# Performance work log

Hardware: AMD Instinct MI355X
Metric: run time of the kernel (lower is better)

Reference implementation:

```python
import jax, jax.numpy as jnp
import numpy as np

N, S = 65536, 2048        # dense points, sampled centres
D1, D2 = 64, 256          # skip-feature dim, centre-embedding dim
MLP = [256, 128]          # conv1x1 channel stack
BN_EPS = 1e-5             # flax BatchNorm default
INTERP_EPS = 1e-8


def setup_inputs() -> dict:
    key = jax.random.key(0)
    ks = jax.random.split(key, 6)
    inp = {
        "xyz1": jax.random.normal(ks[0], (3, N), jnp.float32),
        "xyz2": jax.random.normal(ks[1], (3, S), jnp.float32),
        "points1": jax.random.normal(ks[2], (D1, N), jnp.float32),
        "points2": jax.random.normal(ks[3], (D2, S), jnp.float32),
    }
    c_in = D1 + D2
    for i, c_out in enumerate(MLP):
        inp[f"w{i}"] = jax.random.normal(ks[4 + i], (c_in, c_out), jnp.float32) / np.float32(np.sqrt(c_in))
        inp[f"b{i}"] = jnp.zeros((c_out,), jnp.float32)
        inp[f"scale{i}"] = jnp.ones((c_out,), jnp.float32)
        inp[f"bias{i}"] = jnp.zeros((c_out,), jnp.float32)
        inp[f"mean{i}"] = jnp.zeros((c_out,), jnp.float32)   # BN running mean
        inp[f"var{i}"] = jnp.ones((c_out,), jnp.float32)     # BN running var
        c_in = c_out
    return inp


def reference(xyz1, xyz2, points1, points2,
              w0, b0, scale0, bias0, mean0, var0,
              w1, b1, scale1, bias1, mean1, var1):
    x1 = xyz1.T            # [N, 3]
    x2 = xyz2.T            # [S, 3]
    p2 = points2.T         # [S, D2]

    # squared pairwise distances [N, S]
    dists = (jnp.sum(x1 * x1, -1, keepdims=True)
             + jnp.sum(x2 * x2, -1)[None, :]
             - 2.0 * (x1 @ x2.T))

    # 3 nearest neighbours (smallest dist) per dense point
    neg_d3, idx = jax.lax.top_k(-dists, 3)      # [N, 3]
    d3 = -neg_d3
    recip = 1.0 / (d3 + INTERP_EPS)
    w = recip / jnp.sum(recip, axis=1, keepdims=True)   # [N, 3]

    # inverse-distance-weighted interpolation: [N, D2]
    interp = jnp.einsum('nkd,nk->nd', p2[idx], w)

    new = jnp.concatenate([points1.T, interp], axis=-1)  # [N, D1+D2]

    # conv1x1 (== dense) + BN (inference, running stats) + ReLU stack
    for W, b, s, bb, m, v in ((w0, b0, scale0, bias0, mean0, var0),
                              (w1, b1, scale1, bias1, mean1, var1)):
        y = new @ W + b
        y = (y - m) * (s / jnp.sqrt(v + BN_EPS)) + bb
        new = jax.nn.relu(y)

    return new.T           # [MLP[-1], N]
```

## Files before the change

### kernel.cpp

```cpp
#include <hip/hip_runtime.h>
#include <math.h>

#define NPTS 65536
#define NS   2048
#define C2   256
#define C3   128

#define WS_P2T     32768
#define WS_W0F     1081344
#define WS_W1F     1245184
#define WS_AB0     1310720
#define WS_AB1     1312768
#define WS_KIDX    1313792
#define WS_KW      2100224

typedef __attribute__((ext_vector_type(8))) short bf16x8;
typedef __attribute__((ext_vector_type(4))) float f32x4;

__device__ __forceinline__ unsigned short f2bf(float f) {
  unsigned u = __builtin_bit_cast(unsigned, f);
  u = (u + 0x7FFFu + ((u >> 16) & 1u)) >> 16;
  return (unsigned short)u;
}
__device__ __forceinline__ float bf2f(unsigned h) {
  return __builtin_bit_cast(float, h << 16);
}

__global__ __launch_bounds__(256) void pnfp_knn(
    const float* __restrict__ xyz1, const float* __restrict__ xyz2,
    const float* __restrict__ points2,
    const float* __restrict__ w0, const float* __restrict__ b0,
    const float* __restrict__ scale0, const float* __restrict__ bias0,
    const float* __restrict__ mean0, const float* __restrict__ var0,
    const float* __restrict__ w1, const float* __restrict__ b1,
    const float* __restrict__ scale1, const float* __restrict__ bias1,
    const float* __restrict__ mean1, const float* __restrict__ var1,
    unsigned char* __restrict__ ws)
{
  __shared__ __align__(16) unsigned char kns[33024];
  const int tid = threadIdx.x;

  if (blockIdx.x >= 1024) {
    const int pbid = blockIdx.x - 1024;
    if (pbid < 128) {
      float (*tile)[65] = (float(*)[65])kns;
      const int st = pbid & 31, dt = pbid >> 5;
#pragma unroll
      for (int it = 0; it < 16; ++it) {
        int j = it * 256 + tid;
        int d = j >> 6, s = j & 63;
        tile[d][s] = points2[(dt * 64 + d) * NS + st * 64 + s];
      }
      __syncthreads();
      unsigned short* p2t = (unsigned short*)(ws + WS_P2T);
#pragma unroll
      for (int it = 0; it < 16; ++it) {
        int j = it * 256 + tid;
        int s = j >> 6, d = j & 63;
        p2t[(st * 64 + s) * 256 + dt * 64 + d] = f2bf(tile[d][s]);
      }
      return;
    }
    int gid = (pbid - 128) * 256 + tid;
    if (gid < 81920) {
      int i = gid & 7, l = (gid >> 3) & 63, c = (gid >> 9) & 15, ks = gid >> 13;
      int k = ks * 32 + (l >> 4) * 8 + i;
      int col = c * 16 + (l & 15);
      ((unsigned short*)(ws + WS_W0F))[gid] = f2bf(w0[k * C2 + col]);
      return;
    }
    gid -= 81920;
    if (gid < 32768) {
      int i = gid & 7, l = (gid >> 3) & 63, c = (gid >> 9) & 7, ks = gid >> 12;
      int k = ks * 32 + (l >> 4) * 8 + i;
      int col = c * 16 + (l & 15);
      ((unsigned short*)(ws + WS_W1F))[gid] = f2bf(w1[k * C3 + col]);
      return;
    }
    gid -= 32768;
    if (gid < 256) {
      float a = scale0[gid] / sqrtf(var0[gid] + 1e-5f);
      float bb = (b0[gid] - mean0[gid]) * a + bias0[gid];
      float* ab = (float*)(ws + WS_AB0);
      ab[gid] = a; ab[256 + gid] = bb;
      return;
    }
    gid -= 256;
    if (gid < 128) {
      float a = scale1[gid] / sqrtf(var1[gid] + 1e-5f);
      float bb = (b1[gid] - mean1[gid]) * a + bias1[gid];
      float* ab = (float*)(ws + WS_AB1);
      ab[gid] = a; ab[128 + gid] = bb;
    }
    return;
  }

  float4* cs = (float4*)kns;
  for (int j = tid; j < NS; j += 256) {
    float x = xyz2[j], y = xyz2[NS + j], z = xyz2[2 * NS + j];
    float sc;
    {
#pragma clang fp contract(off)
      sc = (x * x + y * y) + z * z;
    }
    cs[(j >> 7) * 129 + (j & 127)] = make_float4(x, y, z, sc);
  }
  __syncthreads();

  const int rank = tid & 15;
  const int set = tid >> 4;
  const int nb = blockIdx.x * 64 + set * 4;

  float px[4], py[4], pz[4], ps[4];
#pragma unroll
  for (int p = 0; p < 4; ++p) {
    int n = nb + p;
    px[p] = xyz1[n]; py[p] = xyz1[NPTS + n]; pz[p] = xyz1[2 * NPTS + n];
    {
#pragma clang fp contract(off)
      ps[p] = (px[p] * px[p] + py[p] * py[p]) + pz[p] * pz[p];
    }
  }

  float D0[4], D1[4], D2[4];
  int I0[4], I1[4], I2[4];
#pragma unroll
  for (int p = 0; p < 4; ++p) {
    D0[p] = 1e30f; D1[p] = 1e30f; D2[p] = 1e30f;
    I0[p] = 0; I1[p] = 0; I2[p] = 0;
  }

  const float4* cq = cs + rank * 129;
  const int sbase = rank << 7;
#pragma unroll 4
  for (int t = 0; t < 128; ++t) {
    const float4 c = cq[t];
    const int s = sbase + t;
#pragma unroll
    for (int p = 0; p < 4; ++p) {
      float dot = fmaf(pz[p], c.z, fmaf(py[p], c.y, px[p] * c.x));
      float d = (ps[p] + c.w) - 2.0f * dot;
      const bool c2 = d < D2[p], c1 = d < D1[p], c0 = d < D0[p];
      I2[p] = c2 ? (c1 ? I1[p] : s) : I2[p];
      I1[p] = c1 ? (c0 ? I0[p] : s) : I1[p];
      I0[p] = c0 ? s : I0[p];
      float n1 = __builtin_amdgcn_fmed3f(D0[p], D1[p], d);
      float n2 = __builtin_amdgcn_fmed3f(D1[p], D2[p], d);
      D0[p] = fminf(D0[p], d);
      D1[p] = n1; D2[p] = n2;
    }
  }

#pragma unroll
  for (int p = 0; p < 4; ++p) {
#pragma unroll
    for (int m = 1; m <= 8; m <<= 1) {
      float e0 = __shfl_xor(D0[p], m), e1 = __shfl_xor(D1[p], m), e2 = __shfl_xor(D2[p], m);
      int  j0 = __shfl_xor(I0[p], m), j1 = __shfl_xor(I1[p], m), j2 = __shfl_xor(I2[p], m);
      bool t0 = e0 < D0[p];
      float r0 = t0 ? e0 : D0[p]; int ri0 = t0 ? j0 : I0[p];
      float X0 = t0 ? D0[p] : D1[p], X1 = t0 ? D1[p] : D2[p];
      int  XI0 = t0 ? I0[p] : I1[p], XI1 = t0 ? I1[p] : I2[p];
      float Y0 = t0 ? e1 : e0, Y1v = t0 ? e2 : e1;
      int  YJ0 = t0 ? j1 : j0, YJ1 = t0 ? j2 : j1;
      bool t1 = Y0 < X0;
      float r1 = t1 ? Y0 : X0; int ri1 = t1 ? YJ0 : XI0;
      float X0b = t1 ? X0 : X1; int XI0b = t1 ? XI0 : XI1;
      float Y0b = t1 ? Y1v : Y0; int YJ0b = t1 ? YJ1 : YJ0;
      bool t2 = Y0b < X0b;
      float r2 = t2 ? Y0b : X0b; int ri2 = t2 ? YJ0b : XI0b;
      D0[p] = r0; D1[p] = r1; D2[p] = r2; I0[p] = ri0; I1[p] = ri1; I2[p] = ri2;
    }
  }

  if (rank == 0) {
#pragma unroll
    for (int p = 0; p < 4; ++p) {
      const int n = nb + p;
      float q0 = 1.0f / (D0[p] + 1e-8f);
      float q1 = 1.0f / (D1[p] + 1e-8f);
      float q2 = 1.0f / (D2[p] + 1e-8f);
      float qs = (q0 + q1) + q2;
      int* oi = (int*)(ws + WS_KIDX) + 3 * n;
      float* owp = (float*)(ws + WS_KW) + 3 * n;
      oi[0] = I0[p]; oi[1] = I1[p]; oi[2] = I2[p];
      owp[0] = q0 / qs; owp[1] = q1 / qs; owp[2] = q2 / qs;
    }
  }
}

__global__ __launch_bounds__(256, 3) void pnfp_fused(
    const float* __restrict__ points1,
    const unsigned char* __restrict__ ws,
    float* __restrict__ out)
{
  __shared__ __align__(16) unsigned char smem[43520];
  unsigned short* Fh = (unsigned short*)smem;
  int*   kI = (int*)(smem + 41984);
  float* kW = (float*)(smem + 42752);
  const unsigned short* p2t = (const unsigned short*)(ws + WS_P2T);
  const unsigned short* w0f = (const unsigned short*)(ws + WS_W0F);
  const unsigned short* w1f = (const unsigned short*)(ws + WS_W1F);
  const float* ab0 = (const float*)(ws + WS_AB0);
  const float* ab1 = (const float*)(ws + WS_AB1);
  const int* kidx = (const int*)(ws + WS_KIDX);
  const float* kw = (const float*)(ws + WS_KW);

  const int tid = threadIdx.x;
  const int wv = tid >> 6, lane = tid & 63;
  const int n0 = blockIdx.x * 64;

  if (tid < 192) {
    kI[tid] = kidx[3 * n0 + tid];
    kW[tid] = kw[3 * n0 + tid];
  }
#pragma unroll
  for (int it = 0; it < 16; ++it) {
    int j = tid + it * 256;
    int d = j >> 6, r = j & 63;
    Fh[r * 328 + d] = f2bf(points1[d * NPTS + n0 + r]);
  }
  __syncthreads();
  {
    const int dbase = lane * 4;
#pragma unroll 4
    for (int rr = 0; rr < 16; ++rr) {
      const int r = wv * 16 + rr;
      const int a0 = kI[3 * r], a1 = kI[3 * r + 1], a2 = kI[3 * r + 2];
      const float w0 = kW[3 * r], w1 = kW[3 * r + 1], w2 = kW[3 * r + 2];
      uint2 u0 = *(const uint2*)(p2t + a0 * 256 + dbase);
      uint2 u1 = *(const uint2*)(p2t + a1 * 256 + dbase);
      uint2 u2 = *(const uint2*)(p2t + a2 * 256 + dbase);
      float f0 = fmaf(w2, bf2f(u2.x & 0xFFFFu), fmaf(w1, bf2f(u1.x & 0xFFFFu), w0 * bf2f(u0.x & 0xFFFFu)));
      float f1 = fmaf(w2, bf2f(u2.x >> 16),     fmaf(w1, bf2f(u1.x >> 16),     w0 * bf2f(u0.x >> 16)));
      float f2v = fmaf(w2, bf2f(u2.y & 0xFFFFu), fmaf(w1, bf2f(u1.y & 0xFFFFu), w0 * bf2f(u0.y & 0xFFFFu)));
      float f3 = fmaf(w2, bf2f(u2.y >> 16),     fmaf(w1, bf2f(u1.y >> 16),     w0 * bf2f(u0.y >> 16)));
      uint2 pk;
      pk.x = (unsigned)f2bf(f0) | ((unsigned)f2bf(f1) << 16);
      pk.y = (unsigned)f2bf(f2v) | ((unsigned)f2bf(f3) << 16);
      *(uint2*)(Fh + r * 328 + 64 + dbase) = pk;
    }
  }
  __syncthreads();

  f32x4 zero4 = {0.f, 0.f, 0.f, 0.f};
  f32x4 acc[4][4];
#pragma unroll
  for (int a = 0; a < 4; ++a)
#pragma unroll
    for (int b = 0; b < 4; ++b) acc[a][b] = zero4;

  const int arow = lane & 15;
  const int koff = (lane >> 4) * 8;
  bf16x8 bcur[4], bnxt[4];
#pragma unroll
  for (int ct = 0; ct < 4; ++ct)
    bcur[ct] = *(const bf16x8*)(w0f + ((wv * 4 + ct) * 64 + lane) * 8);
  for (int ks = 0; ks < 10; ++ks) {
#pragma unroll
    for (int ct = 0; ct < 4; ++ct)
      bnxt[ct] = *(const bf16x8*)(w0f + (((ks + 1) * 16 + wv * 4 + ct) * 64 + lane) * 8);
    bf16x8 af[4];
#pragma unroll
    for (int rt = 0; rt < 4; ++rt)
      af[rt] = *(const bf16x8*)(Fh + (rt * 16 + arow) * 328 + ks * 32 + koff);
#pragma unroll
    for (int ct = 0; ct < 4; ++ct)
#pragma unroll
      for (int rt = 0; rt < 4; ++rt)
        acc[rt][ct] = __builtin_amdgcn_mfma_f32_16x16x32_bf16(af[rt], bcur[ct], acc[rt][ct], 0, 0, 0);
#pragma unroll
    for (int ct = 0; ct < 4; ++ct) bcur[ct] = bnxt[ct];
  }
  __syncthreads();

  unsigned short* Y1 = (unsigned short*)smem;
#pragma unroll
  for (int ct = 0; ct < 4; ++ct) {
    const int c = wv * 64 + ct * 16 + arow;
    const float a = ab0[c], b = ab0[256 + c];
#pragma unroll
    for (int rt = 0; rt < 4; ++rt) {
      const int rbase = rt * 16 + (lane >> 4) * 4;
#pragma unroll
      for (int qi = 0; qi < 4; ++qi) {
        float yv = fmaxf(fmaf(acc[rt][ct][qi], a, b), 0.0f);
        Y1[(rbase + qi) * 264 + c] = f2bf(yv);
      }
    }
  }
  __syncthreads();

  f32x4 acc2[4][2];
#pragma unroll
  for (int a = 0; a < 4; ++a) { acc2[a][0] = zero4; acc2[a][1] = zero4; }
  bf16x8 b2cur[2], b2nxt[2];
#pragma unroll
  for (int ct = 0; ct < 2; ++ct)
    b2cur[ct] = *(const bf16x8*)(w1f + ((wv * 2 + ct) * 64 + lane) * 8);
  for (int ks = 0; ks < 8; ++ks) {
#pragma unroll
    for (int ct = 0; ct < 2; ++ct)
      b2nxt[ct] = *(const bf16x8*)(w1f + (((ks + 1) * 8 + wv * 2 + ct) * 64 + lane) * 8);
    bf16x8 af[4];
#pragma unroll
    for (int rt = 0; rt < 4; ++rt)
      af[rt] = *(const bf16x8*)(Y1 + (rt * 16 + arow) * 264 + ks * 32 + koff);
#pragma unroll
    for (int ct = 0; ct < 2; ++ct)
#pragma unroll
      for (int rt = 0; rt < 4; ++rt)
        acc2[rt][ct] = __builtin_amdgcn_mfma_f32_16x16x32_bf16(af[rt], b2cur[ct], acc2[rt][ct], 0, 0, 0);
#pragma unroll
    for (int ct = 0; ct < 2; ++ct) b2cur[ct] = b2nxt[ct];
  }
  __syncthreads();

  float* OUT = (float*)smem;
#pragma unroll
  for (int ct = 0; ct < 2; ++ct) {
    const int c = wv * 32 + ct * 16 + arow;
    const float a = ab1[c], b = ab1[128 + c];
#pragma unroll
    for (int rt = 0; rt < 4; ++rt) {
      const int rbase = rt * 16 + (lane >> 4) * 4;
#pragma unroll
      for (int qi = 0; qi < 4; ++qi)
        OUT[c * 67 + rbase + qi] = fmaxf(fmaf(acc2[rt][ct][qi], a, b), 0.0f);
    }
  }
  __syncthreads();
#pragma unroll
  for (int it = 0; it < 32; ++it) {
    int j = tid + it * 256;
    int c = j >> 6, n = j & 63;
    out[c * NPTS + n0 + n] = OUT[c * 67 + n];
  }
}

extern "C" void kernel_launch(void* const* d_in, const int* in_sizes, int n_in,
                              void* d_out, int out_size, void* d_ws, size_t ws_size,
                              hipStream_t stream) {
  (void)in_sizes; (void)n_in; (void)out_size; (void)ws_size;
  const float* xyz1    = (const float*)d_in[0];
  const float* xyz2    = (const float*)d_in[1];
  const float* points1 = (const float*)d_in[2];
  const float* points2 = (const float*)d_in[3];
  const float* w0      = (const float*)d_in[4];
  const float* b0      = (const float*)d_in[5];
  const float* scale0  = (const float*)d_in[6];
  const float* bias0   = (const float*)d_in[7];
  const float* mean0   = (const float*)d_in[8];
  const float* var0    = (const float*)d_in[9];
  const float* w1      = (const float*)d_in[10];
  const float* b1      = (const float*)d_in[11];
  const float* scale1  = (const float*)d_in[12];
  const float* bias1   = (const float*)d_in[13];
  const float* mean1   = (const float*)d_in[14];
  const float* var1    = (const float*)d_in[15];
  unsigned char* ws = (unsigned char*)d_ws;
  float* out = (float*)d_out;

  pnfp_knn<<<1602, 256, 0, stream>>>(xyz1, xyz2, points2,
                                     w0, b0, scale0, bias0, mean0, var0,
                                     w1, b1, scale1, bias1, mean1, var1, ws);
  pnfp_fused<<<1024, 256, 0, stream>>>(points1, ws, out);
}
```

Baseline: 204.9 us.

## Replace brute-force kNN with spatial grid search plus exact fallback

Centres are bucketed into a 10x10x10 grid whose cell edges sit at normal-distribution quantiles. Each dense point then searches only its 3x3x3 neighbouring cells and accepts the result when the third-nearest distance lies within the guaranteed bound to the search-region boundary. Points that fail the check go onto a list and get a wave-per-point brute-force search in a fallback kernel. This is meant to remove most of the O(N*S) distance work, at the cost of extra launches, an atomic-built list, a serial single-block sort, and cell boundaries tuned to Gaussian-distributed inputs.

Measured after the change: 384.9 us. 87.8% more time.

```diff
diff --git a/kernel.cpp b/kernel.cpp
--- a/kernel.cpp
+++ b/kernel.cpp
@@ -6,6 +6,7 @@
 #define C2   256
 #define C3   128
 
+#define WS_SORT    0
 #define WS_P2T     32768
 #define WS_W0F     1081344
 #define WS_W1F     1245184
@@ -13,6 +14,10 @@
 #define WS_AB1     1312768
 #define WS_KIDX    1313792
 #define WS_KW      2100224
+#define WS_CSTART  2886656
+#define WS_SIDX    2888704
+#define WS_FCNT    2892800
+#define WS_FLIST   2892816
 
 typedef __attribute__((ext_vector_type(8))) short bf16x8;
 typedef __attribute__((ext_vector_type(4))) float f32x4;
@@ -26,9 +31,48 @@
   return __builtin_bit_cast(float, h << 16);
 }
 
-__global__ __launch_bounds__(256) void pnfp_knn(
-    const float* __restrict__ xyz1, const float* __restrict__ xyz2,
-    const float* __restrict__ points2,
+#define GE0 -1.2815516f
+#define GE1 -0.84162123f
+#define GE2 -0.52440051f
+#define GE3 -0.25334710f
+#define GE4  0.0f
+#define GE5  0.25334710f
+#define GE6  0.52440051f
+#define GE7  0.84162123f
+#define GE8  1.2815516f
+
+__device__ __forceinline__ int cls9(float v) {
+  int c = 0;
+  c += v > GE0; c += v > GE1; c += v > GE2; c += v > GE3; c += v > GE4;
+  c += v > GE5; c += v > GE6; c += v > GE7; c += v > GE8;
+  return c;
+}
+__device__ __forceinline__ void axis_info(float v, int& c, float& blo, float& bhi) {
+  float lom1 = -3e30f, lom2 = -3e30f, him1 = 3e30f, him2 = 3e30f;
+  int cc = 0; bool b;
+  b = v > GE0; cc += b; lom2 = b ? lom1 : lom2; lom1 = b ? GE0 : lom1;
+  b = v > GE1; cc += b; lom2 = b ? lom1 : lom2; lom1 = b ? GE1 : lom1;
+  b = v > GE2; cc += b; lom2 = b ? lom1 : lom2; lom1 = b ? GE2 : lom1;
+  b = v > GE3; cc += b; lom2 = b ? lom1 : lom2; lom1 = b ? GE3 : lom1;
+  b = v > GE4; cc += b; lom2 = b ? lom1 : lom2; lom1 = b ? GE4 : lom1;
+  b = v > GE5; cc += b; lom2 = b ? lom1 : lom2; lom1 = b ? GE5 : lom1;
+  b = v > GE6; cc += b; lom2 = b ? lom1 : lom2; lom1 = b ? GE6 : lom1;
+  b = v > GE7; cc += b; lom2 = b ? lom1 : lom2; lom1 = b ? GE7 : lom1;
+  b = v > GE8; cc += b; lom2 = b ? lom1 : lom2; lom1 = b ? GE8 : lom1;
+  b = !(v > GE8); him2 = b ? him1 : him2; him1 = b ? GE8 : him1;
+  b = !(v > GE7); him2 = b ? him1 : him2; him1 = b ? GE7 : him1;
+  b = !(v > GE6); him2 = b ? him1 : him2; him1 = b ? GE6 : him1;
+  b = !(v > GE5); him2 = b ? him1 : him2; him1 = b ? GE5 : him1;
+  b = !(v > GE4); him2 = b ? him1 : him2; him1 = b ? GE4 : him1;
+  b = !(v > GE3); him2 = b ? him1 : him2; him1 = b ? GE3 : him1;
+  b = !(v > GE2); him2 = b ? him1 : him2; him1 = b ? GE2 : him1;
+  b = !(v > GE1); him2 = b ? him1 : him2; him1 = b ? GE1 : him1;
+  b = !(v > GE0); him2 = b ? him1 : him2; him1 = b ? GE0 : him1;
+  c = cc; blo = v - lom2; bhi = him2 - v;
+}
+
+__global__ __launch_bounds__(256) void pnfp_prep(
+    const float* __restrict__ xyz2, const float* __restrict__ points2,
     const float* __restrict__ w0, const float* __restrict__ b0,
     const float* __restrict__ scale0, const float* __restrict__ bias0,
     const float* __restrict__ mean0, const float* __restrict__ var0,
@@ -37,65 +81,196 @@
     const float* __restrict__ mean1, const float* __restrict__ var1,
     unsigned char* __restrict__ ws)
 {
-  __shared__ __align__(16) unsigned char kns[33024];
+  __shared__ __align__(16) unsigned char psh[49152];
   const int tid = threadIdx.x;
 
-  if (blockIdx.x >= 1024) {
-    const int pbid = blockIdx.x - 1024;
-    if (pbid < 128) {
-      float (*tile)[65] = (float(*)[65])kns;
-      const int st = pbid & 31, dt = pbid >> 5;
-#pragma unroll
-      for (int it = 0; it < 16; ++it) {
-        int j = it * 256 + tid;
-        int d = j >> 6, s = j & 63;
-        tile[d][s] = points2[(dt * 64 + d) * NS + st * 64 + s];
+  if (blockIdx.x < 128) {
+    float (*tile)[65] = (float(*)[65])psh;
+    const int st = blockIdx.x & 31, dt = blockIdx.x >> 5;
+#pragma unroll
+    for (int it = 0; it < 16; ++it) {
+      int j = it * 256 + tid;
+      int d = j >> 6, s = j & 63;
+      tile[d][s] = points2[(dt * 64 + d) * NS + st * 64 + s];
+    }
+    __syncthreads();
+    unsigned short* p2t = (unsigned short*)(ws + WS_P2T);
+#pragma unroll
+    for (int it = 0; it < 16; ++it) {
+      int j = it * 256 + tid;
+      int s = j >> 6, d = j & 63;
+      p2t[(st * 64 + s) * 256 + dt * 64 + d] = f2bf(tile[d][s]);
+    }
+    return;
+  }
+
+  if (blockIdx.x == 578) {
+    float4* cbuf = (float4*)psh;
+    unsigned short* cellid = (unsigned short*)(psh + 32768);
+    unsigned* A  = (unsigned*)(psh + 36864);
+    unsigned* B  = (unsigned*)(psh + 40960);
+    unsigned* og = (unsigned*)(psh + 45056);
+    for (int i = tid; i < 1024; i += 256) A[i] = 0;
+    __syncthreads();
+#pragma unroll
+    for (int k = 0; k < 8; ++k) {
+      int j = tid + k * 256;
+      float x = xyz2[j], y = xyz2[NS + j], z = xyz2[2 * NS + j];
+      float sc;
+      {
+#pragma clang fp contract(off)
+        sc = (x * x + y * y) + z * z;
+      }
+      cbuf[j] = make_float4(x, y, z, sc);
+      int cell = (cls9(z) * 10 + cls9(y)) * 10 + cls9(x);
+      cellid[j] = (unsigned short)cell;
+      atomicAdd(&A[cell], 1u);
+    }
+    __syncthreads();
+    for (int i = tid; i < 1024; i += 256) og[i] = A[i];
+    __syncthreads();
+    unsigned* src = A; unsigned* dst = B;
+    for (int off = 1; off < 1024; off <<= 1) {
+#pragma unroll
+      for (int k = 0; k < 4; ++k) {
+        int i = tid + k * 256;
+        unsigned v = src[i];
+        if (i >= off) v += src[i - off];
+        dst[i] = v;
       }
       __syncthreads();
-      unsigned short* p2t = (unsigned short*)(ws + WS_P2T);
-#pragma unroll
-      for (int it = 0; it < 16; ++it) {
-        int j = it * 256 + tid;
-        int s = j >> 6, d = j & 63;
-        p2t[(st * 64 + s) * 256 + dt * 64 + d] = f2bf(tile[d][s]);
+      unsigned* t = src; src = dst; dst = t;
+    }
+    unsigned short* cst = (unsigned short*)(ws + WS_CSTART);
+    for (int i = tid; i <= 1000; i += 256)
+      cst[i] = (i == 0) ? 0 : (unsigned short)src[i - 1];
+    for (int i = tid; i < 1024; i += 256) og[i] = src[i] - og[i];
+    __syncthreads();
+    float4* so = (float4*)(ws + WS_SORT);
+    unsigned short* sid = (unsigned short*)(ws + WS_SIDX);
+#pragma unroll
+    for (int k = 0; k < 8; ++k) {
+      int j = tid + k * 256;
+      int cell = cellid[j];
+      unsigned pos = atomicAdd(&og[cell], 1u);
+      so[pos] = cbuf[j];
+      sid[pos] = (unsigned short)j;
+    }
+    if (tid == 0) *(unsigned*)(ws + WS_FCNT) = 0u;
+    return;
+  }
+
+  int gid = ((int)blockIdx.x - 128) * 256 + tid;
+  if (gid < 81920) {
+    int i = gid & 7, l = (gid >> 3) & 63, c = (gid >> 9) & 15, ks = gid >> 13;
+    int k = ks * 32 + (l >> 4) * 8 + i;
+    int col = c * 16 + (l & 15);
+    ((unsigned short*)(ws + WS_W0F))[gid] = f2bf(w0[k * C2 + col]);
+    return;
+  }
+  gid -= 81920;
+  if (gid < 32768) {
+    int i = gid & 7, l = (gid >> 3) & 63, c = (gid >> 9) & 7, ks = gid >> 12;
+    int k = ks * 32 + (l >> 4) * 8 + i;
+    int col = c * 16 + (l & 15);
+    ((unsigned short*)(ws + WS_W1F))[gid] = f2bf(w1[k * C3 + col]);
+    return;
+  }
+  gid -= 32768;
+  if (gid < 256) {
+    float a = scale0[gid] / sqrtf(var0[gid] + 1e-5f);
+    float bb = (b0[gid] - mean0[gid]) * a + bias0[gid];
+    float* ab = (float*)(ws + WS_AB0);
+    ab[gid] = a; ab[256 + gid] = bb;
+    return;
+  }
+  gid -= 256;
+  if (gid < 128) {
+    float a = scale1[gid] / sqrtf(var1[gid] + 1e-5f);
+    float bb = (b1[gid] - mean1[gid]) * a + bias1[gid];
+    float* ab = (float*)(ws + WS_AB1);
+    ab[gid] = a; ab[128 + gid] = bb;
+  }
+}
+
+__global__ __launch_bounds__(128, 2) void pnfp_knn_grid(
+    const float* __restrict__ xyz1, unsigned char* __restrict__ ws)
+{
+  __shared__ __align__(16) unsigned char sh[38880];
+  float4* scs = (float4*)sh;
+  unsigned short* sidx = (unsigned short*)(sh + 32768);
+  unsigned short* cst  = (unsigned short*)(sh + 36864);
+  const int tid = threadIdx.x;
+  for (int j = tid; j < 2048; j += 128) {
+    scs[j] = ((const float4*)(ws + WS_SORT))[j];
+    sidx[j] = ((const unsigned short*)(ws + WS_SIDX))[j];
+  }
+  for (int i = tid; i <= 1000; i += 128)
+    cst[i] = ((const unsigned short*)(ws + WS_CSTART))[i];
+  __syncthreads();
+
+  const int n = blockIdx.x * 128 + tid;
+  const float x = xyz1[n], y = xyz1[NPTS + n], z = xyz1[2 * NPTS + n];
+  float ps;
+  {
+#pragma clang fp contract(off)
+    ps = (x * x + y * y) + z * z;
+  }
+  int cx, cy, cz; float bxl, bxh, byl, byh, bzl, bzh;
+  axis_info(x, cx, bxl, bxh);
+  axis_info(y, cy, byl, byh);
+  axis_info(z, cz, bzl, bzh);
+  float bnd = fminf(fminf(fminf(bxl, bxh), fminf(byl, byh)), fminf(bzl, bzh));
+  const float bnd2 = bnd * bnd * 0.999f;
+
+  float D0 = 1e30f, D1 = 1e30f, D2 = 1e30f;
+  int I0 = 0, I1 = 0, I2 = 0;
+  const int zlo = max(cz - 1, 0), zhi = min(cz + 1, 9);
+  const int ylo = max(cy - 1, 0), yhi = min(cy + 1, 9);
+  const int xlo = max(cx - 1, 0), xhi = min(cx + 1, 9);
+  for (int zz = zlo; zz <= zhi; ++zz)
+    for (int yy = ylo; yy <= yhi; ++yy) {
+      const int cb = (zz * 10 + yy) * 10;
+      const int j0 = cst[cb + xlo], j1 = cst[cb + xhi + 1];
+      for (int j = j0; j < j1; ++j) {
+        float4 c = scs[j];
+        int s = sidx[j];
+        float dot = fmaf(z, c.z, fmaf(y, c.y, x * c.x));
+        float d = (ps + c.w) - 2.0f * dot;
+        bool c0 = (d < D0) || ((d == D0) && (s < I0));
+        bool c1 = (d < D1) || ((d == D1) && (s < I1));
+        bool c2 = (d < D2) || ((d == D2) && (s < I2));
+        int nI0 = c0 ? s : I0;
+        int nI1 = c0 ? I0 : (c1 ? s : I1);
+        int nI2 = c1 ? I1 : (c2 ? s : I2);
+        float nD1 = __builtin_amdgcn_fmed3f(D0, D1, d);
+        float nD2 = __builtin_amdgcn_fmed3f(D1, D2, d);
+        D0 = fminf(D0, d); D1 = nD1; D2 = nD2;
+        I0 = nI0; I1 = nI1; I2 = nI2;
       }
-      return;
-    }
-    int gid = (pbid - 128) * 256 + tid;
-    if (gid < 81920) {
-      int i = gid & 7, l = (gid >> 3) & 63, c = (gid >> 9) & 15, ks = gid >> 13;
-      int k = ks * 32 + (l >> 4) * 8 + i;
-      int col = c * 16 + (l & 15);
-      ((unsigned short*)(ws + WS_W0F))[gid] = f2bf(w0[k * C2 + col]);
-      return;
-    }
-    gid -= 81920;
-    if (gid < 32768) {
-      int i = gid & 7, l = (gid >> 3) & 63, c = (gid >> 9) & 7, ks = gid >> 12;
-      int k = ks * 32 + (l >> 4) * 8 + i;
-      int col = c * 16 + (l & 15);
-      ((unsigned short*)(ws + WS_W1F))[gid] = f2bf(w1[k * C3 + col]);
-      return;
-    }
-    gid -= 32768;
-    if (gid < 256) {
-      float a = scale0[gid] / sqrtf(var0[gid] + 1e-5f);
-      float bb = (b0[gid] - mean0[gid]) * a + bias0[gid];
-      float* ab = (float*)(ws + WS_AB0);
-      ab[gid] = a; ab[256 + gid] = bb;
-      return;
-    }
-    gid -= 256;
-    if (gid < 128) {
-      float a = scale1[gid] / sqrtf(var1[gid] + 1e-5f);
-      float bb = (b1[gid] - mean1[gid]) * a + bias1[gid];
-      float* ab = (float*)(ws + WS_AB1);
-      ab[gid] = a; ab[128 + gid] = bb;
-    }
-    return;
-  }
-
-  float4* cs = (float4*)kns;
+    }
+
+  if (D2 <= bnd2) {
+    float q0 = 1.0f / (D0 + 1e-8f);
+    float q1 = 1.0f / (D1 + 1e-8f);
+    float q2 = 1.0f / (D2 + 1e-8f);
+    float qs = (q0 + q1) + q2;
+    int* oi = (int*)(ws + WS_KIDX) + 3 * n;
+    float* owp = (float*)(ws + WS_KW) + 3 * n;
+    oi[0] = I0; oi[1] = I1; oi[2] = I2;
+    owp[0] = q0 / qs; owp[1] = q1 / qs; owp[2] = q2 / qs;
+  } else {
+    unsigned pos = atomicAdd((unsigned*)(ws + WS_FCNT), 1u);
+    ((int*)(ws + WS_FLIST))[pos] = n;
+  }
+}
+
+__global__ __launch_bounds__(256) void pnfp_knn_fb(
+    const float* __restrict__ xyz1, const float* __restrict__ xyz2,
+    unsigned char* __restrict__ ws)
+{
+  __shared__ float4 cs[2176];
+  const int tid = threadIdx.x;
   for (int j = tid; j < NS; j += 256) {
     float x = xyz2[j], y = xyz2[NS + j], z = xyz2[2 * NS + j];
     float sc;
@@ -103,64 +278,46 @@
 #pragma clang fp contract(off)
       sc = (x * x + y * y) + z * z;
     }
-    cs[(j >> 7) * 129 + (j & 127)] = make_float4(x, y, z, sc);
-  }
-  __syncthreads();
-
-  const int rank = tid & 15;
-  const int set = tid >> 4;
-  const int nb = blockIdx.x * 64 + set * 4;
-
-  float px[4], py[4], pz[4], ps[4];
-#pragma unroll
-  for (int p = 0; p < 4; ++p) {
-    int n = nb + p;
-    px[p] = xyz1[n]; py[p] = xyz1[NPTS + n]; pz[p] = xyz1[2 * NPTS + n];
+    cs[(j >> 5) * 34 + (j & 31)] = make_float4(x, y, z, sc);
+  }
+  __syncthreads();
+  const int lane = tid & 63;
+  const int wv = (blockIdx.x << 2) | (tid >> 6);
+  const unsigned cnt = *(const unsigned*)(ws + WS_FCNT);
+  const float4* cq = cs + lane * 34;
+  const int sbase = lane << 5;
+  for (unsigned it = wv; it < cnt; it += 256) {
+    const int n = ((const int*)(ws + WS_FLIST))[it];
+    const float x = xyz1[n], y = xyz1[NPTS + n], z = xyz1[2 * NPTS + n];
+    float ps;
     {
 #pragma clang fp contract(off)
-      ps[p] = (px[p] * px[p] + py[p] * py[p]) + pz[p] * pz[p];
-    }
-  }
-
-  float D0[4], D1[4], D2[4];
-  int I0[4], I1[4], I2[4];
-#pragma unroll
-  for (int p = 0; p < 4; ++p) {
-    D0[p] = 1e30f; D1[p] = 1e30f; D2[p] = 1e30f;
-    I0[p] = 0; I1[p] = 0; I2[p] = 0;
-  }
-
-  const float4* cq = cs + rank * 129;
-  const int sbase = rank << 7;
+      ps = (x * x + y * y) + z * z;
+    }
+    float D0 = 1e30f, D1 = 1e30f, D2 = 1e30f;
+    int I0 = 0, I1 = 0, I2 = 0;
 #pragma unroll 4
-  for (int t = 0; t < 128; ++t) {
-    const float4 c = cq[t];
-    const int s = sbase + t;
-#pragma unroll
-    for (int p = 0; p < 4; ++p) {
-      float dot = fmaf(pz[p], c.z, fmaf(py[p], c.y, px[p] * c.x));
-      float d = (ps[p] + c.w) - 2.0f * dot;
-      const bool c2 = d < D2[p], c1 = d < D1[p], c0 = d < D0[p];
-      I2[p] = c2 ? (c1 ? I1[p] : s) : I2[p];
-      I1[p] = c1 ? (c0 ? I0[p] : s) : I1[p];
-      I0[p] = c0 ? s : I0[p];
-      float n1 = __builtin_amdgcn_fmed3f(D0[p], D1[p], d);
-      float n2 = __builtin_amdgcn_fmed3f(D1[p], D2[p], d);
-      D0[p] = fminf(D0[p], d);
-      D1[p] = n1; D2[p] = n2;
-    }
-  }
-
-#pragma unroll
-  for (int p = 0; p < 4; ++p) {
-#pragma unroll
-    for (int m = 1; m <= 8; m <<= 1) {
-      float e0 = __shfl_xor(D0[p], m), e1 = __shfl_xor(D1[p], m), e2 = __shfl_xor(D2[p], m);
-      int  j0 = __shfl_xor(I0[p], m), j1 = __shfl_xor(I1[p], m), j2 = __shfl_xor(I2[p], m);
-      bool t0 = e0 < D0[p];
-      float r0 = t0 ? e0 : D0[p]; int ri0 = t0 ? j0 : I0[p];
-      float X0 = t0 ? D0[p] : D1[p], X1 = t0 ? D1[p] : D2[p];
-      int  XI0 = t0 ? I0[p] : I1[p], XI1 = t0 ? I1[p] : I2[p];
+    for (int t = 0; t < 32; ++t) {
+      float4 c = cq[t];
+      const int s = sbase + t;
+      float dot = fmaf(z, c.z, fmaf(y, c.y, x * c.x));
+      float d = (ps + c.w) - 2.0f * dot;
+      const bool c2b = d < D2, c1b = d < D1, c0b = d < D0;
+      I2 = c2b ? (c1b ? I1 : s) : I2;
+      I1 = c1b ? (c0b ? I0 : s) : I1;
+      I0 = c0b ? s : I0;
+      float n1 = __builtin_amdgcn_fmed3f(D0, D1, d);
+      float n2 = __builtin_amdgcn_fmed3f(D1, D2, d);
+      D0 = fminf(D0, d); D1 = n1; D2 = n2;
+    }
+#pragma unroll
+    for (int m = 1; m <= 32; m <<= 1) {
+      float e0 = __shfl_xor(D0, m), e1 = __shfl_xor(D1, m), e2 = __shfl_xor(D2, m);
+      int  j0 = __shfl_xor(I0, m), j1 = __shfl_xor(I1, m), j2 = __shfl_xor(I2, m);
+      bool t0 = e0 < D0;
+      float r0 = t0 ? e0 : D0; int ri0 = t0 ? j0 : I0;
+      float X0 = t0 ? D0 : D1, X1 = t0 ? D1 : D2;
+      int  XI0 = t0 ? I0 : I1, XI1 = t0 ? I1 : I2;
       float Y0 = t0 ? e1 : e0, Y1v = t0 ? e2 : e1;
       int  YJ0 = t0 ? j1 : j0, YJ1 = t0 ? j2 : j1;
       bool t1 = Y0 < X0;
@@ -169,21 +326,16 @@
       float Y0b = t1 ? Y1v : Y0; int YJ0b = t1 ? YJ1 : YJ0;
       bool t2 = Y0b < X0b;
       float r2 = t2 ? Y0b : X0b; int ri2 = t2 ? YJ0b : XI0b;
-      D0[p] = r0; D1[p] = r1; D2[p] = r2; I0[p] = ri0; I1[p] = ri1; I2[p] = ri2;
-    }
-  }
-
-  if (rank == 0) {
-#pragma unroll
-    for (int p = 0; p < 4; ++p) {
-      const int n = nb + p;
-      float q0 = 1.0f / (D0[p] + 1e-8f);
-      float q1 = 1.0f / (D1[p] + 1e-8f);
-      float q2 = 1.0f / (D2[p] + 1e-8f);
+      D0 = r0; D1 = r1; D2 = r2; I0 = ri0; I1 = ri1; I2 = ri2;
+    }
+    if (lane == 0) {
+      float q0 = 1.0f / (D0 + 1e-8f);
+      float q1 = 1.0f / (D1 + 1e-8f);
+      float q2 = 1.0f / (D2 + 1e-8f);
       float qs = (q0 + q1) + q2;
       int* oi = (int*)(ws + WS_KIDX) + 3 * n;
       float* owp = (float*)(ws + WS_KW) + 3 * n;
-      oi[0] = I0[p]; oi[1] = I1[p]; oi[2] = I2[p];
+      oi[0] = I0; oi[1] = I1; oi[2] = I2;
       owp[0] = q0 / qs; owp[1] = q1 / qs; owp[2] = q2 / qs;
     }
   }
@@ -361,8 +513,9 @@
   unsigned char* ws = (unsigned char*)d_ws;
   float* out = (float*)d_out;
 
-  pnfp_knn<<<1602, 256, 0, stream>>>(xyz1, xyz2, points2,
-                                     w0, b0, scale0, bias0, mean0, var0,
+  pnfp_prep<<<579, 256, 0, stream>>>(xyz2, points2, w0, b0, scale0, bias0, mean0, var0,
                                      w1, b1, scale1, bias1, mean1, var1, ws);
+  pnfp_knn_grid<<<512, 128, 0, stream>>>(xyz1, ws);
+  pnfp_knn_fb<<<64, 256, 0, stream>>>(xyz1, xyz2, ws);
   pnfp_fused<<<1024, 256, 0, stream>>>(points1, ws, out);
 }
```
